# Kernel tuning notes

Hardware: AMD Instinct MI355X
Metric: run time of the kernel (lower is better)

Reference implementation:

```python
import jax, jax.numpy as jnp
import numpy as np

BATCH = 4_194_304

def _invariants(F):
    # F: (b,3,3). C = F^T F. Invariants [tr(C), det(F), -det(F), I2]
    C = jnp.einsum('bji,bjk->bik', F, F)
    trC = jnp.trace(C, axis1=-2, axis2=-1)
    trC2 = jnp.einsum('bij,bji->b', C, C)
    I2 = 0.5 * (trC * trC - trC2)
    J = jnp.linalg.det(F)
    return jnp.stack([trC, J, -J, I2], axis=-1)  # (b,4)

def _mlp(x, W0, b0, Wh, bh, Wf, bf):
    h = jax.nn.softplus(x @ W0 + b0)
    for i in range(Wh.shape[0]):  # fixed small layer count
        h = jax.nn.softplus(h @ Wh[i] + bh[i])
    return jax.nn.softplus(h @ Wf + bf)  # (b,1)

def setup_inputs() -> dict:
    key = jax.random.key(0)
    ks = jax.random.split(key, 4)
    # deformation gradients near identity
    F = jnp.eye(3, dtype=jnp.float32)[None] + 0.1 * jax.random.normal(ks[0], (BATCH, 3, 3), dtype=jnp.float32)
    # NonNeg-constrained kernels -> uniform [0,1)
    W0 = jax.random.uniform(ks[1], (4, 5), dtype=jnp.float32)
    b0 = jnp.zeros((5,), jnp.float32)
    Wh = jax.random.uniform(ks[2], (4, 5, 5), dtype=jnp.float32)
    bh = jnp.zeros((4, 5), jnp.float32)
    Wf = jax.random.uniform(ks[3], (5, 1), dtype=jnp.float32)
    bf = jnp.zeros((1,), jnp.float32)
    return {"F": F, "W0": W0, "b0": b0, "Wh": Wh, "bh": bh, "Wf": Wf, "bf": bf}

def reference(F, W0, b0, Wh, bh, Wf, bf):
    energy = _mlp(_invariants(F), W0, b0, Wh, bh, Wf, bf)  # (b,1)

    # energy at identity and its gradient wrt identity F (same for all samples)
    def e_id(Fi):
        return _mlp(_invariants(Fi[None]), W0, b0, Wh, bh, Wf, bf)[0, 0]
    eye = jnp.eye(3, dtype=F.dtype)
    energy_identity, gI = jax.value_and_grad(e_id)(eye)
    H = -gI  # (3,3), broadcast over batch

    # Green-Lagrange strain E = (F^T F - I)/2
    C = jnp.einsum('bji,bjk->bik', F, F)
    E = 0.5 * (C - eye)
    correction = jnp.einsum('ij,bij->b', H, E)[:, None]  # (b,1)
    return energy - energy_identity + correction
```

## Files before the change

### kernel.cpp

```cpp
#include <hip/hip_runtime.h>
#include <math.h>

typedef float v4 __attribute__((ext_vector_type(4)));
typedef float v2 __attribute__((ext_vector_type(2)));

__device__ __forceinline__ float spf(float x) {
    float a = fabsf(x);
    float e = __expf(-a);
    float l = __logf(1.0f + e);
    return fmaxf(x, 0.0f) + l;
}
__device__ __forceinline__ float spn(float x) {
    return __logf(1.0f + __expf(x));
}
__device__ __forceinline__ float sigm(float x) {
    return 1.0f / (1.0f + __expf(-x));
}
__device__ __forceinline__ v4 splat(float s) { v4 r; r.x=s; r.y=s; r.z=s; r.w=s; return r; }
__device__ __forceinline__ v4 sp4(v4 x) {
    v4 r; r.x=spf(x.x); r.y=spf(x.y); r.z=spf(x.z); r.w=spf(x.w); return r;
}
__device__ __forceinline__ v4 sp4n(v4 x) {
    v4 r; r.x=spn(x.x); r.y=spn(x.y); r.z=spn(x.z); r.w=spn(x.w); return r;
}
__device__ __forceinline__ v4 spq4(v4 x) {
    v4 r;
    r.x = x.x + __expf(-x.x);
    r.y = x.y + __expf(-x.y);
    r.z = x.z + __expf(-x.z);
    r.w = x.w + __expf(-x.w);
    return r;
}
__device__ __forceinline__ v4 vfma(v4 a, float b, v4 c) {
    v2 bb; bb.x = b; bb.y = b;
    v4 r;
    r.lo = __builtin_elementwise_fma(a.lo, bb, c.lo);
    r.hi = __builtin_elementwise_fma(a.hi, bb, c.hi);
    return r;
}
__device__ __forceinline__ v4 vmin(v4 a, v4 b) {
    v4 r; r.x=fminf(a.x,b.x); r.y=fminf(a.y,b.y); r.z=fminf(a.z,b.z); r.w=fminf(a.w,b.w); return r;
}

__global__ void setup_kernel(const float* __restrict__ W0, const float* __restrict__ b0,
                             const float* __restrict__ Wh, const float* __restrict__ bh,
                             const float* __restrict__ Wf, const float* __restrict__ bf,
                             float* __restrict__ ws) {
    if (threadIdx.x != 0 || blockIdx.x != 0) return;
    float x[4] = {3.f, 1.f, -1.f, 3.f};
    float zin[5], h[5], zh[4][5];
    for (int j = 0; j < 5; ++j) {
        float z = b0[j];
        for (int m = 0; m < 4; ++m) z += x[m] * W0[m * 5 + j];
        zin[j] = z; h[j] = spf(z);
    }
    for (int i = 0; i < 4; ++i) {
        float hn[5];
        for (int j = 0; j < 5; ++j) {
            float z = bh[i * 5 + j];
            for (int k = 0; k < 5; ++k) z += h[k] * Wh[i * 25 + k * 5 + j];
            zh[i][j] = z; hn[j] = spf(z);
        }
        for (int j = 0; j < 5; ++j) h[j] = hn[j];
    }
    float zf = bf[0];
    for (int k = 0; k < 5; ++k) zf += h[k] * Wf[k];
    float e_id = spf(zf);
    float d[5];
    float szf = sigm(zf);
    for (int k = 0; k < 5; ++k) d[k] = Wf[k] * szf;
    for (int i = 3; i >= 0; --i) {
        float dz[5];
        for (int j = 0; j < 5; ++j) dz[j] = d[j] * sigm(zh[i][j]);
        for (int k = 0; k < 5; ++k) {
            float acc = 0.f;
            for (int j = 0; j < 5; ++j) acc += Wh[i * 25 + k * 5 + j] * dz[j];
            d[k] = acc;
        }
    }
    float dz0[5], g[4];
    for (int j = 0; j < 5; ++j) dz0[j] = d[j] * sigm(zin[j]);
    for (int m = 0; m < 4; ++m) {
        float acc = 0.f;
        for (int j = 0; j < 5; ++j) acc += W0[m * 5 + j] * dz0[j];
        g[m] = acc;
    }
    float h_s = -(2.f * g[0] + g[1] - g[2] + 4.f * g[3]);
    ws[0] = e_id;
    ws[1] = h_s;
}

__device__ __forceinline__ float scalar_sample(const float* f,
        const float* W0, const float* b0, const float* Wh, const float* bh,
        const float* Wf, const float* bf, float e_id, float h_s) {
    float f0=f[0],f1=f[1],f2=f[2],f3=f[3],f4=f[4],f5=f[5],f6=f[6],f7=f[7],f8=f[8];
    float c00=f0*f0+f3*f3+f6*f6, c11=f1*f1+f4*f4+f7*f7, c22=f2*f2+f5*f5+f8*f8;
    float c01=f0*f1+f3*f4+f6*f7, c02=f0*f2+f3*f5+f6*f8, c12=f1*f2+f4*f5+f7*f8;
    float trC=c00+c11+c22;
    float trC2=c00*c00+c11*c11+c22*c22+2.f*(c01*c01+c02*c02+c12*c12);
    float I2=0.5f*(trC*trC-trC2);
    float J=f0*(f4*f8-f5*f7)-f1*(f3*f8-f5*f6)+f2*(f3*f7-f4*f6);
    float h[5];
    for (int j=0;j<5;++j)
        h[j]=spf(b0[j]+trC*W0[j]+J*(W0[5+j]-W0[10+j])+I2*W0[15+j]);
    for (int l=0;l<4;++l){
        float hn[5];
        for (int j=0;j<5;++j){
            float z=bh[l*5+j];
            for (int k=0;k<5;++k) z=fmaf(h[k],Wh[l*25+k*5+j],z);
            hn[j]=spf(z);
        }
        for (int j=0;j<5;++j) h[j]=hn[j];
    }
    float zf=bf[0];
    for (int k=0;k<5;++k) zf=fmaf(h[k],Wf[k],zf);
    return (spf(zf)-e_id)+h_s*0.5f*(trC-3.0f);
}

__device__ __forceinline__ void inv9(
        float f0, float f1, float f2, float f3, float f4,
        float f5, float f6, float f7, float f8,
        float& tc_o, float& J_o, float& I2_o) {
    float c00=f0*f0+f3*f3+f6*f6, c11=f1*f1+f4*f4+f7*f7, c22=f2*f2+f5*f5+f8*f8;
    float c01=f0*f1+f3*f4+f6*f7, c02=f0*f2+f3*f5+f6*f8, c12=f1*f2+f4*f5+f7*f8;
    float tc=c00+c11+c22;
    float trC2=c00*c00+c11*c11+c22*c22+2.f*(c01*c01+c02*c02+c12*c12);
    tc_o=tc;
    I2_o=0.5f*(tc*tc-trC2);
    J_o=f0*(f4*f8-f5*f7)-f1*(f3*f8-f5*f6)+f2*(f3*f7-f4*f6);
}

__global__ __launch_bounds__(256, 8) void main_kernel(
        const float* __restrict__ F,
        const float* __restrict__ W0, const float* __restrict__ b0,
        const float* __restrict__ Wh, const float* __restrict__ bh,
        const float* __restrict__ Wf, const float* __restrict__ bf,
        const float* __restrict__ cs,
        float* __restrict__ out, int n) {
    const long long t = (long long)blockIdx.x * blockDim.x + threadIdx.x;
    const long long i0 = t * 4;
    if (i0 >= n) return;
    const float eid = cs[0], hs = cs[1];

    if (i0 + 4 <= (long long)n) {
        const v4* p = (const v4*)(F + i0 * 9);
        v4 a0=p[0],a1=p[1],a2=p[2],a3=p[3],a4=p[4],a5=p[5],a6=p[6],a7=p[7],a8=p[8];

        float tc0,j0,q0, tc1,j1,q1, tc2,j2,q2, tc3,j3,q3;
        inv9(a0.x,a0.y,a0.z,a0.w, a1.x,a1.y,a1.z,a1.w, a2.x, tc0,j0,q0);
        inv9(a2.y,a2.z,a2.w, a3.x,a3.y,a3.z,a3.w, a4.x,a4.y, tc1,j1,q1);
        inv9(a4.z,a4.w, a5.x,a5.y,a5.z,a5.w, a6.x,a6.y,a6.z, tc2,j2,q2);
        inv9(a6.w, a7.x,a7.y,a7.z,a7.w, a8.x,a8.y,a8.z,a8.w, tc3,j3,q3);
        v4 trC, J, I2;
        trC.x=tc0; trC.y=tc1; trC.z=tc2; trC.w=tc3;
        J.x=j0; J.y=j1; J.z=j2; J.w=j3;
        I2.x=q0; I2.y=q1; I2.z=q2; I2.w=q3;

        v4 h0,h1,h2,h3,h4;
        {
            v4 z;
            #define L0(J_, H_) \
                z = splat(b0[J_]); \
                z = vfma(trC, W0[J_], z); \
                z = vfma(J, W0[5+J_]-W0[10+J_], z); \
                z = vfma(I2, W0[15+J_], z); \
                H_ = sp4n(z);
            L0(0,h0) L0(1,h1) L0(2,h2) L0(3,h3) L0(4,h4)
            #undef L0
        }
        #pragma unroll
        for (int l = 0; l < 4; ++l) {
            v4 z0,z1,z2,z3,z4;
            #define ZJ(J_, Z_) \
                Z_ = splat(bh[l*5+J_]); \
                Z_ = vfma(h0, Wh[l*25+0*5+J_], Z_); \
                Z_ = vfma(h1, Wh[l*25+1*5+J_], Z_); \
                Z_ = vfma(h2, Wh[l*25+2*5+J_], Z_); \
                Z_ = vfma(h3, Wh[l*25+3*5+J_], Z_); \
                Z_ = vfma(h4, Wh[l*25+4*5+J_], Z_);
            ZJ(0,z0) ZJ(1,z1) ZJ(2,z2) ZJ(3,z3) ZJ(4,z4)
            #undef ZJ
            v4 m = vmin(vmin(vmin(z0,z1),vmin(z2,z3)),z4);
            float mm = fminf(fminf(m.x,m.y),fminf(m.z,m.w));
            if (__all(mm > 17.0f)) {
                h0=z0; h1=z1; h2=z2; h3=z3; h4=z4;
            } else if (__all(mm > 2.0f)) {
                h0=spq4(z0); h1=spq4(z1); h2=spq4(z2); h3=spq4(z3); h4=spq4(z4);
            } else {
                h0=sp4(z0); h1=sp4(z1); h2=sp4(z2); h3=sp4(z3); h4=sp4(z4);
            }
        }
        v4 zf = splat(bf[0]);
        zf = vfma(h0, Wf[0], zf);
        zf = vfma(h1, Wf[1], zf);
        zf = vfma(h2, Wf[2], zf);
        zf = vfma(h3, Wf[3], zf);
        zf = vfma(h4, Wf[4], zf);
        float mf = fminf(fminf(zf.x, zf.y), fminf(zf.z, zf.w));
        v4 e;
        if (__all(mf > 17.0f)) e = zf;
        else if (__all(mf > 2.0f)) e = spq4(zf);
        else e = sp4(zf);

        v4 res = (e - splat(eid)) + splat(hs * 0.5f) * (trC - splat(3.0f));
        *(v4*)(out + i0) = res;
    } else {
        for (int s = 0; s < (int)(n - i0); ++s)
            out[i0 + s] = scalar_sample(F + (size_t)(i0 + s) * 9, W0, b0, Wh, bh, Wf, bf, eid, hs);
    }
}

extern "C" void kernel_launch(void* const* d_in, const int* in_sizes, int n_in,
                              void* d_out, int out_size, void* d_ws, size_t ws_size,
                              hipStream_t stream) {
    const float* F  = (const float*)d_in[0];
    const float* W0 = (const float*)d_in[1];
    const float* b0 = (const float*)d_in[2];
    const float* Wh = (const float*)d_in[3];
    const float* bh = (const float*)d_in[4];
    const float* Wf = (const float*)d_in[5];
    const float* bf = (const float*)d_in[6];
    float* out = (float*)d_out;
    float* ws  = (float*)d_ws;
    int n = in_sizes[0] / 9;
    setup_kernel<<<1, 64, 0, stream>>>(W0, b0, Wh, bh, Wf, bf, ws);
    int block = 256;
    long long threads = ((long long)n + 3) / 4;
    int grid = (int)((threads + block - 1) / block);
    if (grid < 1) grid = 1;
    main_kernel<<<grid, block, 0, stream>>>(F, W0, b0, Wh, bh, Wf, bf, ws, out, n);
}
```

Baseline: 51.70 us.

## Fuse identity-energy setup into main kernel and add fast path for first layer

Removes the separate single-thread setup kernel and instead has the first wavefront of every block recompute the identity energy and gradient constants, sharing them through shared memory after a block barrier. This drops one kernel launch and the serialized dependency between the two launches. The cost is redundant per-block work, a __syncthreads, and dropping the occupancy hint from launch bounds. It also adds a wave-uniform cheaper softplus branch for the first layer and folds the constants into a single fma at output.

Result: slower. 55.04 us (+6.5%).

```diff
diff --git a/kernel.cpp b/kernel.cpp
--- a/kernel.cpp
+++ b/kernel.cpp
@@ -40,54 +40,6 @@
 }
 __device__ __forceinline__ v4 vmin(v4 a, v4 b) {
     v4 r; r.x=fminf(a.x,b.x); r.y=fminf(a.y,b.y); r.z=fminf(a.z,b.z); r.w=fminf(a.w,b.w); return r;
-}
-
-__global__ void setup_kernel(const float* __restrict__ W0, const float* __restrict__ b0,
-                             const float* __restrict__ Wh, const float* __restrict__ bh,
-                             const float* __restrict__ Wf, const float* __restrict__ bf,
-                             float* __restrict__ ws) {
-    if (threadIdx.x != 0 || blockIdx.x != 0) return;
-    float x[4] = {3.f, 1.f, -1.f, 3.f};
-    float zin[5], h[5], zh[4][5];
-    for (int j = 0; j < 5; ++j) {
-        float z = b0[j];
-        for (int m = 0; m < 4; ++m) z += x[m] * W0[m * 5 + j];
-        zin[j] = z; h[j] = spf(z);
-    }
-    for (int i = 0; i < 4; ++i) {
-        float hn[5];
-        for (int j = 0; j < 5; ++j) {
-            float z = bh[i * 5 + j];
-            for (int k = 0; k < 5; ++k) z += h[k] * Wh[i * 25 + k * 5 + j];
-            zh[i][j] = z; hn[j] = spf(z);
-        }
-        for (int j = 0; j < 5; ++j) h[j] = hn[j];
-    }
-    float zf = bf[0];
-    for (int k = 0; k < 5; ++k) zf += h[k] * Wf[k];
-    float e_id = spf(zf);
-    float d[5];
-    float szf = sigm(zf);
-    for (int k = 0; k < 5; ++k) d[k] = Wf[k] * szf;
-    for (int i = 3; i >= 0; --i) {
-        float dz[5];
-        for (int j = 0; j < 5; ++j) dz[j] = d[j] * sigm(zh[i][j]);
-        for (int k = 0; k < 5; ++k) {
-            float acc = 0.f;
-            for (int j = 0; j < 5; ++j) acc += Wh[i * 25 + k * 5 + j] * dz[j];
-            d[k] = acc;
-        }
-    }
-    float dz0[5], g[4];
-    for (int j = 0; j < 5; ++j) dz0[j] = d[j] * sigm(zin[j]);
-    for (int m = 0; m < 4; ++m) {
-        float acc = 0.f;
-        for (int j = 0; j < 5; ++j) acc += W0[m * 5 + j] * dz0[j];
-        g[m] = acc;
-    }
-    float h_s = -(2.f * g[0] + g[1] - g[2] + 4.f * g[3]);
-    ws[0] = e_id;
-    ws[1] = h_s;
 }
 
 __device__ __forceinline__ float scalar_sample(const float* f,
@@ -101,18 +53,24 @@
     float I2=0.5f*(trC*trC-trC2);
     float J=f0*(f4*f8-f5*f7)-f1*(f3*f8-f5*f6)+f2*(f3*f7-f4*f6);
     float h[5];
+    #pragma unroll
     for (int j=0;j<5;++j)
         h[j]=spf(b0[j]+trC*W0[j]+J*(W0[5+j]-W0[10+j])+I2*W0[15+j]);
+    #pragma unroll
     for (int l=0;l<4;++l){
         float hn[5];
+        #pragma unroll
         for (int j=0;j<5;++j){
             float z=bh[l*5+j];
+            #pragma unroll
             for (int k=0;k<5;++k) z=fmaf(h[k],Wh[l*25+k*5+j],z);
             hn[j]=spf(z);
         }
+        #pragma unroll
         for (int j=0;j<5;++j) h[j]=hn[j];
     }
     float zf=bf[0];
+    #pragma unroll
     for (int k=0;k<5;++k) zf=fmaf(h[k],Wf[k],zf);
     return (spf(zf)-e_id)+h_s*0.5f*(trC-3.0f);
 }
@@ -130,19 +88,80 @@
     J_o=f0*(f4*f8-f5*f7)-f1*(f3*f8-f5*f6)+f2*(f3*f7-f4*f6);
 }
 
-__global__ __launch_bounds__(256, 8) void main_kernel(
+__global__ __launch_bounds__(256) void main_kernel(
         const float* __restrict__ F,
         const float* __restrict__ W0, const float* __restrict__ b0,
         const float* __restrict__ Wh, const float* __restrict__ bh,
         const float* __restrict__ Wf, const float* __restrict__ bf,
-        const float* __restrict__ cs,
         float* __restrict__ out, int n) {
-    const long long t = (long long)blockIdx.x * blockDim.x + threadIdx.x;
+    __shared__ float s_c[2];
+    const int tid = threadIdx.x;
+    const long long t = (long long)blockIdx.x * blockDim.x + tid;
     const long long i0 = t * 4;
-    if (i0 >= n) return;
-    const float eid = cs[0], hs = cs[1];
-
-    if (i0 + 4 <= (long long)n) {
+
+    if (tid < 64) {
+        float x[4] = {3.f, 1.f, -1.f, 3.f};
+        float zin[5], h[5], zh[4][5];
+        #pragma unroll
+        for (int j = 0; j < 5; ++j) {
+            float z = b0[j];
+            #pragma unroll
+            for (int m = 0; m < 4; ++m) z += x[m] * W0[m * 5 + j];
+            zin[j] = z; h[j] = spf(z);
+        }
+        #pragma unroll
+        for (int i = 0; i < 4; ++i) {
+            float hn[5];
+            #pragma unroll
+            for (int j = 0; j < 5; ++j) {
+                float z = bh[i * 5 + j];
+                #pragma unroll
+                for (int k = 0; k < 5; ++k) z += h[k] * Wh[i * 25 + k * 5 + j];
+                zh[i][j] = z; hn[j] = spf(z);
+            }
+            #pragma unroll
+            for (int j = 0; j < 5; ++j) h[j] = hn[j];
+        }
+        float zf = bf[0];
+        #pragma unroll
+        for (int k = 0; k < 5; ++k) zf += h[k] * Wf[k];
+        float e_id = spf(zf);
+        float d[5];
+        float szf = sigm(zf);
+        #pragma unroll
+        for (int k = 0; k < 5; ++k) d[k] = Wf[k] * szf;
+        #pragma unroll
+        for (int i = 3; i >= 0; --i) {
+            float dz[5];
+            #pragma unroll
+            for (int j = 0; j < 5; ++j) dz[j] = d[j] * sigm(zh[i][j]);
+            #pragma unroll
+            for (int k = 0; k < 5; ++k) {
+                float acc = 0.f;
+                #pragma unroll
+                for (int j = 0; j < 5; ++j) acc += Wh[i * 25 + k * 5 + j] * dz[j];
+                d[k] = acc;
+            }
+        }
+        float dz0[5], g[4];
+        #pragma unroll
+        for (int j = 0; j < 5; ++j) dz0[j] = d[j] * sigm(zin[j]);
+        #pragma unroll
+        for (int m = 0; m < 4; ++m) {
+            float acc = 0.f;
+            #pragma unroll
+            for (int j = 0; j < 5; ++j) acc += W0[m * 5 + j] * dz0[j];
+            g[m] = acc;
+        }
+        float h_s = -(2.f * g[0] + g[1] - g[2] + 4.f * g[3]);
+        float c1 = 0.5f * h_s;
+        float c0 = -e_id - 3.0f * c1;
+        if (tid == 0) { s_c[0] = c0; s_c[1] = c1; }
+    }
+
+    const bool full = (i0 + 4 <= (long long)n);
+    v4 e = splat(0.0f), trC = splat(0.0f);
+    if (full) {
         const v4* p = (const v4*)(F + i0 * 9);
         v4 a0=p[0],a1=p[1],a2=p[2],a3=p[3],a4=p[4],a5=p[5],a6=p[6],a7=p[7],a8=p[8];
 
@@ -151,22 +170,28 @@
         inv9(a2.y,a2.z,a2.w, a3.x,a3.y,a3.z,a3.w, a4.x,a4.y, tc1,j1,q1);
         inv9(a4.z,a4.w, a5.x,a5.y,a5.z,a5.w, a6.x,a6.y,a6.z, tc2,j2,q2);
         inv9(a6.w, a7.x,a7.y,a7.z,a7.w, a8.x,a8.y,a8.z,a8.w, tc3,j3,q3);
-        v4 trC, J, I2;
+        v4 J, I2;
         trC.x=tc0; trC.y=tc1; trC.z=tc2; trC.w=tc3;
         J.x=j0; J.y=j1; J.z=j2; J.w=j3;
         I2.x=q0; I2.y=q1; I2.z=q2; I2.w=q3;
 
         v4 h0,h1,h2,h3,h4;
         {
-            v4 z;
-            #define L0(J_, H_) \
-                z = splat(b0[J_]); \
-                z = vfma(trC, W0[J_], z); \
-                z = vfma(J, W0[5+J_]-W0[10+J_], z); \
-                z = vfma(I2, W0[15+J_], z); \
-                H_ = sp4n(z);
-            L0(0,h0) L0(1,h1) L0(2,h2) L0(3,h3) L0(4,h4)
-            #undef L0
+            v4 z0,z1,z2,z3,z4;
+            #define L0Z(J_, Z_) \
+                Z_ = splat(b0[J_]); \
+                Z_ = vfma(trC, W0[J_], Z_); \
+                Z_ = vfma(J, W0[5+J_]-W0[10+J_], Z_); \
+                Z_ = vfma(I2, W0[15+J_], Z_);
+            L0Z(0,z0) L0Z(1,z1) L0Z(2,z2) L0Z(3,z3) L0Z(4,z4)
+            #undef L0Z
+            v4 m = vmin(vmin(vmin(z0,z1),vmin(z2,z3)),z4);
+            float mm = fminf(fminf(m.x,m.y),fminf(m.z,m.w));
+            if (__all(mm > 2.0f)) {
+                h0=spq4(z0); h1=spq4(z1); h2=spq4(z2); h3=spq4(z3); h4=spq4(z4);
+            } else {
+                h0=sp4n(z0); h1=sp4n(z1); h2=sp4n(z2); h3=sp4n(z3); h4=sp4n(z4);
+            }
         }
         #pragma unroll
         for (int l = 0; l < 4; ++l) {
@@ -197,16 +222,23 @@
         zf = vfma(h3, Wf[3], zf);
         zf = vfma(h4, Wf[4], zf);
         float mf = fminf(fminf(zf.x, zf.y), fminf(zf.z, zf.w));
-        v4 e;
         if (__all(mf > 17.0f)) e = zf;
         else if (__all(mf > 2.0f)) e = spq4(zf);
         else e = sp4(zf);
-
-        v4 res = (e - splat(eid)) + splat(hs * 0.5f) * (trC - splat(3.0f));
+    }
+
+    __syncthreads();
+    const float c0 = s_c[0], c1 = s_c[1];
+
+    if (full) {
+        v4 res = (e + splat(c0)) + splat(c1) * trC;
         *(v4*)(out + i0) = res;
-    } else {
+    } else if (i0 < (long long)n) {
+        float c1v = c1;
+        float h_s = 2.0f * c1v;
+        float e_id = -c0 - 3.0f * c1v;
         for (int s = 0; s < (int)(n - i0); ++s)
-            out[i0 + s] = scalar_sample(F + (size_t)(i0 + s) * 9, W0, b0, Wh, bh, Wf, bf, eid, hs);
+            out[i0 + s] = scalar_sample(F + (size_t)(i0 + s) * 9, W0, b0, Wh, bh, Wf, bf, e_id, h_s);
     }
 }
 
@@ -221,12 +253,10 @@
     const float* Wf = (const float*)d_in[5];
     const float* bf = (const float*)d_in[6];
     float* out = (float*)d_out;
-    float* ws  = (float*)d_ws;
     int n = in_sizes[0] / 9;
-    setup_kernel<<<1, 64, 0, stream>>>(W0, b0, Wh, bh, Wf, bf, ws);
     int block = 256;
     long long threads = ((long long)n + 3) / 4;
     int grid = (int)((threads + block - 1) / block);
     if (grid < 1) grid = 1;
-    main_kernel<<<grid, block, 0, stream>>>(F, W0, b0, Wh, bh, Wf, bf, ws, out, n);
-}
+    main_kernel<<<grid, block, 0, stream>>>(F, W0, b0, Wh, bh, Wf, bf, out, n);
+}
```

## Stage F loads through LDS with coalesced global_load_lds per wave

Applied to the files above, without the earlier changes.

Replaces each thread's strided 9×16-byte loads of F with wave-cooperative, fully coalesced global_load_lds transfers into shared memory. Each thread then reads its own 36 floats back from LDS. The goal is better global memory coalescing on this bandwidth-bound kernel. In exchange it uses 36 KB of LDS per block and drops the occupancy hint from launch_bounds, which may lower occupancy, and the per-thread LDS reads with a 9-v4 stride may hit bank conflicts.

New measurement: 53.25 us. 3.0% more time.

```diff
diff --git a/kernel.cpp b/kernel.cpp
--- a/kernel.cpp
+++ b/kernel.cpp
@@ -130,21 +130,42 @@
     J_o=f0*(f4*f8-f5*f7)-f1*(f3*f8-f5*f6)+f2*(f3*f7-f4*f6);
 }
 
-__global__ __launch_bounds__(256, 8) void main_kernel(
+__global__ __launch_bounds__(256) void main_kernel(
         const float* __restrict__ F,
         const float* __restrict__ W0, const float* __restrict__ b0,
         const float* __restrict__ Wh, const float* __restrict__ bh,
         const float* __restrict__ Wf, const float* __restrict__ bf,
         const float* __restrict__ cs,
         float* __restrict__ out, int n) {
-    const long long t = (long long)blockIdx.x * blockDim.x + threadIdx.x;
+    __shared__ v4 lds4[4 * 576];
+    const int tid  = threadIdx.x;
+    const int wave = tid >> 6;
+    const int lane = tid & 63;
+    const long long t = (long long)blockIdx.x * 256 + tid;
     const long long i0 = t * 4;
-    if (i0 >= n) return;
+    const long long samp0 = ((long long)blockIdx.x * 4 + wave) * 256;
     const float eid = cs[0], hs = cs[1];
 
-    if (i0 + 4 <= (long long)n) {
-        const v4* p = (const v4*)(F + i0 * 9);
-        v4 a0=p[0],a1=p[1],a2=p[2],a3=p[3],a4=p[4],a5=p[5],a6=p[6],a7=p[7],a8=p[8];
+    if (samp0 + 256 <= (long long)n) {
+        const float* gbase = F + samp0 * 9;
+        v4* lw = lds4 + wave * 576;
+        #pragma unroll
+        for (int c = 0; c < 9; ++c) {
+            const float* gp = gbase + (size_t)(c * 64 + lane) * 4;
+            __builtin_amdgcn_global_load_lds(
+                (const __attribute__((address_space(1))) void*)gp,
+                (__attribute__((address_space(3))) void*)(lw + c * 64),
+                16, 0, 0);
+        }
+        asm volatile("s_waitcnt vmcnt(0)" ::: "memory");
+        __builtin_amdgcn_sched_barrier(0);
+
+        v4 a0,a1,a2,a3,a4,a5,a6,a7,a8;
+        {
+            const v4* mine = lw + 9 * lane;
+            a0=mine[0]; a1=mine[1]; a2=mine[2]; a3=mine[3]; a4=mine[4];
+            a5=mine[5]; a6=mine[6]; a7=mine[7]; a8=mine[8];
+        }
 
         float tc0,j0,q0, tc1,j1,q1, tc2,j2,q2, tc3,j3,q3;
         inv9(a0.x,a0.y,a0.z,a0.w, a1.x,a1.y,a1.z,a1.w, a2.x, tc0,j0,q0);
@@ -204,8 +225,8 @@
 
         v4 res = (e - splat(eid)) + splat(hs * 0.5f) * (trC - splat(3.0f));
         *(v4*)(out + i0) = res;
-    } else {
-        for (int s = 0; s < (int)(n - i0); ++s)
+    } else if (i0 < (long long)n) {
+        for (int s = 0; s < (int)(n - i0) && s < 4; ++s)
             out[i0 + s] = scalar_sample(F + (size_t)(i0 + s) * 9, W0, b0, Wh, bh, Wf, bf, eid, hs);
     }
 }
```
